# Kernel optimization log

Measured on AMD Instinct MI355X. Metric: run time of the kernel, lower is better.

Reference implementation:

```python
import jax, jax.numpy as jnp
import numpy as np
from jax import lax

H = 384
W = 384
N = H * W                 # flattened pixel count
N_LOC = N // 2            # unknown pixels with 3x3 matting-Laplacian stencils
KCM = 20                  # color-mixture KNN size
K_IU = 5                  # intra-unknown KNN size
NNZ_CM = N_LOC * KCM


def setup_inputs() -> dict:
    key = jax.random.key(0)
    ks = jax.random.split(key, 16)
    f32 = jnp.float32
    i32 = jnp.int32
    inp = {}
    inp["CM_weights"] = jax.random.uniform(ks[0], (N,), f32)
    inp["LOC_weights"] = jax.random.uniform(ks[1], (N,), f32)
    inp["IU_weights"] = jax.random.uniform(ks[2], (N,), f32)
    inp["KU_weights"] = jax.random.uniform(ks[3], (N,), f32)
    inp["lmbda"] = jnp.full((1,), 100.0, f32)
    inp["kToUconf"] = jax.random.uniform(ks[4], (N,), f32)
    inp["known"] = jax.random.uniform(ks[5], (N,), f32)
    inp["kToU"] = jax.random.uniform(ks[6], (N,), f32)
    inp["Wcm_data"] = jax.random.uniform(ks[7], (NNZ_CM,), f32)
    inp["LOC_flows"] = jax.random.uniform(ks[8], (9, 9, N_LOC), f32)
    inp["IU_flows"] = jax.random.uniform(ks[9], (N_LOC, K_IU), f32)
    inp["Wcm_row"] = jax.random.randint(ks[10], (NNZ_CM,), 0, N, dtype=i32)
    inp["Wcm_col"] = jax.random.randint(ks[11], (NNZ_CM,), 0, N, dtype=i32)
    # interior pixels so all 9 stencil neighbours are valid
    inp["LOC_inInd"] = jax.random.randint(ks[12], (N_LOC,), W + 1, N - W - 1, dtype=i32)
    inp["IU_inInd"] = jax.random.randint(ks[13], (N_LOC,), 0, N, dtype=i32)
    inp["IU_neighInd"] = jax.random.randint(ks[14], (N_LOC, K_IU), 0, N, dtype=i32)
    inp["width"] = W
    inp["cg_steps"] = 30
    return inp


def reference(CM_weights, LOC_weights, IU_weights, KU_weights, lmbda,
              kToUconf, known, kToU, Wcm_data, LOC_flows, IU_flows,
              Wcm_row, Wcm_col, LOC_inInd, IU_inInd, IU_neighInd,
              width, cg_steps):
    n = kToU.shape[0]
    seg = lambda v, i: jax.ops.segment_sum(v, i, num_segments=n)

    # --- color mixture: Wcm scaled by diag(CM_weights); L = diag(rowsum) - Wcm; Lcm = L^T L
    cm_vals = CM_weights[Wcm_row] * Wcm_data
    rs_cm = seg(cm_vals, Wcm_row)

    # --- matting Laplacian: 9x9 flows per unknown pixel over 3x3 stencil
    offs = jnp.array([-1 - width, -1, -1 + width, -width, 0, width,
                      1 - width, 1, 1 + width], dtype=LOC_inInd.dtype)
    neigh = LOC_inInd[:, None] + offs[None, :]                    # [n_loc, 9]
    fl = LOC_flows * LOC_weights[LOC_inInd][None, None, :]        # [9, 9, n_loc]
    nloc = neigh.shape[0]
    # entry (row=neigh[k,i], col=neigh[k,j]) has value fl[j, i, k]
    vals_m = jnp.transpose(fl, (2, 1, 0)).reshape(-1)
    rows_m = jnp.broadcast_to(neigh[:, :, None], (nloc, 9, 9)).reshape(-1)
    cols_m = jnp.broadcast_to(neigh[:, None, :], (nloc, 9, 9)).reshape(-1)
    rows_ms = jnp.concatenate([rows_m, cols_m])
    cols_ms = jnp.concatenate([cols_m, rows_m])
    vals_ms = 0.5 * jnp.concatenate([vals_m, vals_m])             # W = 0.5 (W + W^T)
    rs_m = seg(vals_ms, rows_ms)

    # --- intra-unknowns KNN affinities
    fiu = IU_flows * IU_weights[IU_inInd][:, None]                # [n_iu, K]
    rows_c0 = jnp.broadcast_to(IU_inInd[:, None], IU_neighInd.shape).reshape(-1)
    cols_c0 = IU_neighInd.reshape(-1)
    rows_cs = jnp.concatenate([rows_c0, cols_c0])
    cols_cs = jnp.concatenate([cols_c0, rows_c0])
    vals_cs = 0.5 * jnp.concatenate([fiu.reshape(-1), fiu.reshape(-1)])
    rs_c = seg(vals_cs, rows_cs)

    # --- diagonal data terms: KU + lmbda*known
    diag_ku = KU_weights * kToUconf + lmbda[0] * known
    b = diag_ku * kToU

    def matvec(v):
        # Lcm @ v = L^T (L v), keeping L in factored COO form
        Lv = rs_cm * v - seg(cm_vals * v[Wcm_col], Wcm_row)
        lcm = rs_cm * Lv - seg(cm_vals * Lv[Wcm_row], Wcm_col)
        lm = rs_m * v - seg(vals_ms * v[cols_ms], rows_ms)
        lc = rs_c * v - seg(vals_cs * v[cols_cs], rows_cs)
        return lcm + lm + lc + diag_ku * v

    def cg_step(carry, _):
        x, r, p, rs = carry
        Ap = matvec(p)
        alpha = rs / jnp.vdot(p, Ap)
        x = x + alpha * p
        r = r - alpha * Ap
        rs_new = jnp.vdot(r, r)
        p = r + (rs_new / rs) * p
        return (x, r, p, rs_new), None

    x0 = jnp.zeros_like(b)  # x0 = 0 as in MattingSolver
    (x, _, _, _), _ = lax.scan(cg_step, (x0, b, b, jnp.vdot(b, b)), None, length=cg_steps)
    return x
```

## Files before the change

### kernel.cpp

```cpp
#include <hip/hip_runtime.h>


#define TPB 256

__device__ __forceinline__ float blockReduce256(float v) {
  #pragma unroll
  for (int o = 32; o > 0; o >>= 1) v += __shfl_down(v, o, 64);
  __shared__ float s[4];
  int lane = threadIdx.x & 63, wv = threadIdx.x >> 6;
  if (lane == 0) s[wv] = v;
  __syncthreads();
  return (threadIdx.x == 0) ? (s[0] + s[1] + s[2] + s[3]) : 0.f;
}

__global__ void k_init0(const float* __restrict__ KUw, const float* __restrict__ kToUconf,
                        const float* __restrict__ lmbda, const float* __restrict__ known,
                        const float* __restrict__ kToU,
                        float* __restrict__ diag_ku, float2* __restrict__ PR,
                        float* __restrict__ x,
                        int* __restrict__ CNT, float* __restrict__ scal, int N)
{
  int i = blockIdx.x * TPB + threadIdx.x;
  if (i < 80) scal[i] = 0.f;
  if (i < 4 * N) CNT[i] = 0;
  float red = 0.f;
  if (i < N) {
    float dk = KUw[i] * kToUconf[i] + lmbda[0] * known[i];
    diag_ku[i] = dk;
    float b = dk * kToU[i];
    PR[i] = make_float2(b, b);
    x[i] = 0.f;
    red = b * b;
  }
  float v = blockReduce256(red);
  if (threadIdx.x == 0) atomicAdd(&scal[0], v);
}

__global__ void k_prep(float* __restrict__ LOC_flows, const int* __restrict__ LOC_inInd,
                       const float* __restrict__ LOCw, int NLOC)
{
  int k = blockIdx.x * TPB + threadIdx.x;
  float Fl[81];
  #pragma unroll
  for (int m = 0; m < 81; ++m) Fl[m] = LOC_flows[(size_t)m * NLOC + k];
  float hw = 0.5f * LOCw[LOC_inInd[k]];
  int idx = 0;
  #pragma unroll
  for (int a = 0; a < 9; ++a)
    #pragma unroll
    for (int b = a + 1; b < 9; ++b) {
      LOC_flows[(size_t)idx * NLOC + k] = hw * (Fl[a * 9 + b] + Fl[b * 9 + a]);
      ++idx;
    }
}

__global__ void k_sh(const int* __restrict__ LOC_inInd, int* __restrict__ CNT,
                     unsigned short* __restrict__ sTick, int N, int NLOC)
{
  int k = blockIdx.x * TPB + threadIdx.x;
  sTick[k] = (unsigned short)atomicAdd(&CNT[3 * N + LOC_inInd[k]], 1);
}

__global__ void k_sc(const int* __restrict__ LOC_inInd, const int* __restrict__ OFF,
                     const unsigned short* __restrict__ sTick,
                     int* __restrict__ perm, int* __restrict__ LOC_inIndP,
                     int N, int NLOC)
{
  int k = blockIdx.x * TPB + threadIdx.x;
  int v = LOC_inInd[k];
  int pos = OFF[3 * N + v] + sTick[k];
  perm[pos] = k;
  LOC_inIndP[pos] = v;
}

__global__ void k_permS2(float* __restrict__ LOC_flows, const int* __restrict__ perm,
                         int NLOC)
{
  int kp = blockIdx.x * TPB + threadIdx.x;
  int k = perm[kp];
  #pragma unroll
  for (int m = 0; m < 36; ++m)
    LOC_flows[(size_t)(36 + m) * NLOC + kp] = LOC_flows[(size_t)m * NLOC + k];
}

__global__ void k_hist(const int* __restrict__ Wrow, const int* __restrict__ Wcol,
                       const int* __restrict__ IU_inInd, const int* __restrict__ IU_neighInd,
                       int* __restrict__ CNT,
                       unsigned short* __restrict__ tr, unsigned short* __restrict__ tc,
                       unsigned short* __restrict__ tU,
                       int NLOC, int N, int B0)
{
  int blk = blockIdx.x;
  if (blk < B0) {
    int e = blk * TPB + threadIdx.x;
    tr[e] = (unsigned short)atomicAdd(&CNT[Wrow[e]], 1);
    tc[e] = (unsigned short)atomicAdd(&CNT[N + Wcol[e]], 1);
  } else {
    int k = (blk - B0) * TPB + threadIdx.x;
    tU[5 * NLOC + k] = (unsigned short)atomicAdd(&CNT[2 * N + IU_inInd[k]], 1);
    #pragma unroll
    for (int j = 0; j < 5; ++j)
      tU[j * NLOC + k] =
          (unsigned short)atomicAdd(&CNT[2 * N + IU_neighInd[k * 5 + j]], 1);
  }
}

__global__ void k_scan1(int* __restrict__ OFF, int* __restrict__ bsum, int tot)
{
  __shared__ int s[TPB];
  int gid = blockIdx.x * TPB + threadIdx.x;
  int v = (gid < tot) ? OFF[gid] : 0;
  s[threadIdx.x] = v;
  __syncthreads();
  #pragma unroll
  for (int o = 1; o < TPB; o <<= 1) {
    int t = (threadIdx.x >= o) ? s[threadIdx.x - o] : 0;
    __syncthreads();
    s[threadIdx.x] += t;
    __syncthreads();
  }
  if (gid < tot) OFF[gid] = s[threadIdx.x] - v;
  if (threadIdx.x == TPB - 1) bsum[blockIdx.x] = s[threadIdx.x];
}

__global__ void k_scan2(int* __restrict__ bsum, int nPerArr)
{
  __shared__ int s[1024];
  int base = blockIdx.x * nPerArr;
  int v = (threadIdx.x < nPerArr) ? bsum[base + threadIdx.x] : 0;
  s[threadIdx.x] = v;
  __syncthreads();
  for (int o = 1; o < 1024; o <<= 1) {
    int t = (threadIdx.x >= o) ? s[threadIdx.x - o] : 0;
    __syncthreads();
    s[threadIdx.x] += t;
    __syncthreads();
  }
  if (threadIdx.x < nPerArr) bsum[base + threadIdx.x] = s[threadIdx.x] - v;
}

__global__ void k_scan3(int* __restrict__ OFF, const int* __restrict__ bsum, int tot)
{
  int gid = blockIdx.x * TPB + threadIdx.x;
  if (gid < tot) OFF[gid] += bsum[blockIdx.x];
}

__global__ void k_fill(const float* __restrict__ CMw, const float* __restrict__ Wcm_data,
                       const int* __restrict__ Wrow, const int* __restrict__ Wcol,
                       const int* __restrict__ IU_inInd, const int* __restrict__ IU_neighInd,
                       const int* __restrict__ OFF,
                       const unsigned short* __restrict__ tr, const unsigned short* __restrict__ tc,
                       const unsigned short* __restrict__ tU,
                       int2* __restrict__ csrPk, int2* __restrict__ cscPk,
                       int* __restrict__ gU,
                       int NLOC, int N, int B0)
{
  int blk = blockIdx.x;
  if (blk < B0) {
    int e = blk * TPB + threadIdx.x;
    int row = Wrow[e], col = Wcol[e];
    int cv = __float_as_int(CMw[row] * Wcm_data[e]);
    csrPk[OFF[row] + tr[e]] = make_int2(col, cv);
    cscPk[OFF[N + col] + tc[e]] = make_int2(row, cv);
  } else {
    int k = (blk - B0) * TPB + threadIdx.x;
    gU[OFF[2 * N + IU_inInd[k]] + tU[5 * NLOC + k]] = 14 * NLOC + k;
    #pragma unroll
    for (int j = 0; j < 5; ++j)
      gU[OFF[2 * N + IU_neighInd[k * 5 + j]] + tU[j * NLOC + k]] =
          (9 + j) * NLOC + k;
  }
}

__global__ void k_it1(const float2* __restrict__ PR,
                      const float* __restrict__ S2p, const int* __restrict__ LOC_inIndP,
                      const int* __restrict__ width_p,
                      const float* __restrict__ IU_flows, const int* __restrict__ IU_inInd,
                      const int* __restrict__ IU_neighInd, const float* __restrict__ IUw,
                      const float* __restrict__ diag_ku,
                      const int* __restrict__ OFF, const int2* __restrict__ csrPk,
                      float* __restrict__ u_all,
                      float* __restrict__ Lv, float* __restrict__ rs_cm,
                      const float* __restrict__ rsN, const float* __restrict__ rsO, int first,
                      float* __restrict__ pAp_t,
                      int NNZ, int NLOC, int N, int B0, int B1)
{
  int blk = blockIdx.x;
  float beta = first ? 0.f : rsN[0] / rsO[0];
  float red = 0.f;
  if (blk < B0) {
    int kp = blk * TPB + threadIdx.x;
    int wd = *width_p;
    int base = LOC_inIndP[kp];
    const int offs[9] = {-1 - wd, -1, -1 + wd, -wd, 0, wd, 1 - wd, 1, 1 + wd};
    float pv[9];
    #pragma unroll
    for (int a = 0; a < 9; ++a) {
      float2 pr = PR[base + offs[a]];
      pv[a] = __builtin_fmaf(beta, pr.x, pr.y);
    }
    float u[9] = {0.f, 0.f, 0.f, 0.f, 0.f, 0.f, 0.f, 0.f, 0.f};
    float qf = 0.f;
    int idx = 0;
    #pragma unroll
    for (int a = 0; a < 9; ++a)
      #pragma unroll
      for (int b = a + 1; b < 9; ++b) {
        float sv = S2p[(size_t)idx * NLOC + kp];
        ++idx;
        float d = pv[a] - pv[b];
        float t = sv * d;
        u[a] += t; u[b] -= t;
        qf += t * d;
      }
    #pragma unroll
    for (int a = 0; a < 9; ++a) u_all[a * NLOC + kp] = u[a];
    red = qf;
  } else if (blk < B1) {
    int k = (blk - B0) * TPB + threadIdx.x;
    int r0 = IU_inInd[k];
    float hw = 0.5f * IUw[r0];
    float2 prr = PR[r0];
    float pr = __builtin_fmaf(beta, prr.x, prr.y);
    int c[5]; float w[5];
    #pragma unroll
    for (int j = 0; j < 5; ++j) {
      c[j] = IU_neighInd[k * 5 + j];
      w[j] = hw * IU_flows[k * 5 + j];
    }
    float pc[5];
    #pragma unroll
    for (int j = 0; j < 5; ++j) {
      float2 pp = PR[c[j]];
      pc[j] = __builtin_fmaf(beta, pp.x, pp.y);
    }
    float qf = 0.f, asum = 0.f;
    #pragma unroll
    for (int j = 0; j < 5; ++j) {
      float d = pr - pc[j];
      float uA = w[j] * d;
      u_all[(9 + j) * NLOC + k] = -uA;
      asum += uA;
      qf += uA * d;
    }
    u_all[14 * NLOC + k] = asum;
    red = qf;
  } else {
    int i = (blk - B1) * TPB + threadIdx.x;
    float2 pri = PR[i];
    float pi = __builtin_fmaf(beta, pri.x, pri.y);
    int s = OFF[i];
    int e = (i == N - 1) ? NNZ : OFF[i + 1];
    float acc = 0.f, rs = 0.f;
    int q = s;
    for (; q + 8 <= e; q += 8) {
      int2 ed[8];
      #pragma unroll
      for (int m = 0; m < 8; ++m) ed[m] = csrPk[q + m];
      float g[8];
      #pragma unroll
      for (int m = 0; m < 8; ++m) {
        float2 pp = PR[ed[m].x];
        g[m] = __builtin_fmaf(beta, pp.x, pp.y);
      }
      #pragma unroll
      for (int m = 0; m < 8; ++m) {
        float cv = __int_as_float(ed[m].y);
        rs += cv;
        acc += cv * (pi - g[m]);
      }
    }
    for (; q + 4 <= e; q += 4) {
      int2 ed[4];
      #pragma unroll
      for (int m = 0; m < 4; ++m) ed[m] = csrPk[q + m];
      float g[4];
      #pragma unroll
      for (int m = 0; m < 4; ++m) {
        float2 pp = PR[ed[m].x];
        g[m] = __builtin_fmaf(beta, pp.x, pp.y);
      }
      #pragma unroll
      for (int m = 0; m < 4; ++m) {
        float cv = __int_as_float(ed[m].y);
        rs += cv;
        acc += cv * (pi - g[m]);
      }
    }
    for (; q < e; ++q) {
      int2 ed = csrPk[q];
      float cv = __int_as_float(ed.y);
      float2 pp = PR[ed.x];
      rs += cv;
      acc += cv * (pi - __builtin_fmaf(beta, pp.x, pp.y));
    }
    Lv[i] = acc;
    rs_cm[i] = rs;
    red = diag_ku[i] * pi * pi + acc * acc;
  }
  float v = blockReduce256(red);
  if (threadIdx.x == 0) atomicAdd(pAp_t, v);
}

__global__ void k_it2(float* __restrict__ x, float2* __restrict__ PR,
                      const float* __restrict__ Lv,
                      const float* __restrict__ rs_cm, const float* __restrict__ diag_ku,
                      const int* __restrict__ OFF, const int* __restrict__ cum,
                      const int* __restrict__ width_p,
                      const int2* __restrict__ cscPk,
                      const int* __restrict__ gU, const float* __restrict__ u_all,
                      const float* __restrict__ rs_t, const float* __restrict__ pAp_t,
                      const float* __restrict__ rsO, int first,
                      float* __restrict__ rs_t1,
                      int NNZ, int NLOC, int N)
{
  int i = blockIdx.x * TPB + threadIdx.x;
  float alpha = rs_t[0] / pAp_t[0];
  float beta = first ? 0.f : rs_t[0] / rsO[0];
  float tg = 0.f;
  {
    int wd = *width_p;
    const int voff[9] = {1 + wd, 1, 1 - wd, wd, 0, -wd, -1 + wd, -1, -1 - wd};
    #pragma unroll
    for (int a = 0; a < 9; ++a) {
      int v = i + voff[a];
      v = v < 0 ? 0 : (v > N - 1 ? N - 1 : v);
      int lo = cum[v];
      int hi = (v == N - 1) ? NLOC : cum[v + 1];
      for (int q = lo; q < hi; ++q) tg += u_all[a * NLOC + q];
    }
  }
  {
    int s0 = OFF[2 * N + i];
    int e0 = (i == N - 1) ? 6 * NLOC : OFF[2 * N + i + 1];
    int q = s0;
    for (; q + 4 <= e0; q += 4) {
      int g[4];
      #pragma unroll
      for (int m = 0; m < 4; ++m) g[m] = gU[q + m];
      float u[4];
      #pragma unroll
      for (int m = 0; m < 4; ++m) u[m] = u_all[g[m]];
      #pragma unroll
      for (int m = 0; m < 4; ++m) tg += u[m];
    }
    for (; q < e0; ++q) tg += u_all[gU[q]];
  }
  float sc = 0.f;
  {
    int s0 = OFF[N + i];
    int e0 = (i == N - 1) ? NNZ : OFF[N + i + 1];
    int q = s0;
    for (; q + 8 <= e0; q += 8) {
      int2 ed[8];
      #pragma unroll
      for (int m = 0; m < 8; ++m) ed[m] = cscPk[q + m];
      float l[8];
      #pragma unroll
      for (int m = 0; m < 8; ++m) l[m] = Lv[ed[m].x];
      #pragma unroll
      for (int m = 0; m < 8; ++m) sc += __int_as_float(ed[m].y) * l[m];
    }
    for (; q + 4 <= e0; q += 4) {
      int2 ed[4];
      #pragma unroll
      for (int m = 0; m < 4; ++m) ed[m] = cscPk[q + m];
      float l[4];
      #pragma unroll
      for (int m = 0; m < 4; ++m) l[m] = Lv[ed[m].x];
      #pragma unroll
      for (int m = 0; m < 4; ++m) sc += __int_as_float(ed[m].y) * l[m];
    }
    for (; q < e0; ++q) {
      int2 ed = cscPk[q];
      sc += __int_as_float(ed.y) * Lv[ed.x];
    }
  }
  float2 pri = PR[i];
  float pi = __builtin_fmaf(beta, pri.x, pri.y);
  float Ap = diag_ku[i] * pi + rs_cm[i] * Lv[i] - sc + tg;
  x[i] += alpha * pi;
  float rn = pri.y - alpha * Ap;
  PR[i] = make_float2(pi, rn);
  float v = blockReduce256(rn * rn);
  if (threadIdx.x == 0) atomicAdd(rs_t1, v);
}

extern "C" void kernel_launch(void* const* d_in, const int* in_sizes, int n_in,
                              void* d_out, int out_size, void* d_ws, size_t ws_size,
                              hipStream_t stream)
{
  const float* CMw       = (const float*)d_in[0];
  const float* LOCw      = (const float*)d_in[1];
  const float* IUw       = (const float*)d_in[2];
  const float* KUw       = (const float*)d_in[3];
  const float* lmbda     = (const float*)d_in[4];
  const float* kToUconf  = (const float*)d_in[5];
  const float* known     = (const float*)d_in[6];
  const float* kToU      = (const float*)d_in[7];
  const float* Wcm_data  = (const float*)d_in[8];
  float*       LOC_flows = (float*)d_in[9];
  const float* IU_flows  = (const float*)d_in[10];
  const int*   Wrow      = (const int*)d_in[11];
  const int*   Wcol      = (const int*)d_in[12];
  const int*   LOC_inInd = (const int*)d_in[13];
  const int*   IU_inInd  = (const int*)d_in[14];
  const int*   IU_neighInd = (const int*)d_in[15];
  const int*   width_p   = (const int*)d_in[16];
  const int CG_STEPS = 30;

  const int N    = in_sizes[0];
  const int NNZ  = in_sizes[8];
  const int NLOC = in_sizes[13];

  float* x       = (float*)d_out;
  float2* PR     = (float2*)d_ws;
  float* Lv      = (float*)(PR + (size_t)N);
  float* rs_cm   = Lv + N;
  float* diag_ku = rs_cm + N;
  int2*  csrPk   = (int2*)(diag_ku + N);
  int2*  cscPk   = csrPk + (size_t)NNZ;
  int*   gU      = (int*)(cscPk + (size_t)NNZ);
  int*   OFF     = gU + (size_t)6 * NLOC;
  unsigned short* tr = (unsigned short*)(OFF + (size_t)4 * N);
  unsigned short* tc = tr + (size_t)NNZ;
  unsigned short* tU = tc + (size_t)NNZ;
  float* u_all   = (float*)tr;
  int*   bsum    = (int*)(tU + (size_t)6 * NLOC);
  float* scal    = (float*)(bsum + 4 * (N / TPB));
  int*   perm    = (int*)(scal + 80);
  int*   LOC_inIndP = perm + NLOC;
  unsigned short* sTick = (unsigned short*)(LOC_inIndP + NLOC);

  const int Bn = N / TPB;
  const int Bz = NNZ / TPB;
  const int Bl = NLOC / TPB;
  const int Z4 = 4 * Bn;

  k_init0<<<Z4, TPB, 0, stream>>>(KUw, kToUconf, lmbda, known, kToU,
                                  diag_ku, PR, x, OFF, scal, N);
  k_prep<<<Bl, TPB, 0, stream>>>(LOC_flows, LOC_inInd, LOCw, NLOC);
  k_sh<<<Bl, TPB, 0, stream>>>(LOC_inInd, OFF, sTick, N, NLOC);
  k_hist<<<Bz + Bl, TPB, 0, stream>>>(Wrow, Wcol, IU_inInd, IU_neighInd, OFF,
                                      tr, tc, tU, NLOC, N, Bz);
  k_scan1<<<Z4, TPB, 0, stream>>>(OFF, bsum, 4 * N);
  k_scan2<<<4, 1024, 0, stream>>>(bsum, Bn);
  k_scan3<<<Z4, TPB, 0, stream>>>(OFF, bsum, 4 * N);
  k_sc<<<Bl, TPB, 0, stream>>>(LOC_inInd, OFF, sTick, perm, LOC_inIndP, N, NLOC);
  k_permS2<<<Bl, TPB, 0, stream>>>(LOC_flows, perm, NLOC);
  k_fill<<<Bz + Bl, TPB, 0, stream>>>(CMw, Wcm_data, Wrow, Wcol,
                                      IU_inInd, IU_neighInd,
                                      OFF, tr, tc, tU,
                                      csrPk, cscPk, gU,
                                      NLOC, N, Bz);

  const float* S2p = LOC_flows + (size_t)36 * NLOC;
  const int*   cum = OFF + (size_t)3 * N;
  for (int t = 0; t < CG_STEPS; ++t) {
    const float* rsN = scal + t;
    const float* rsO = scal + (t == 0 ? 0 : t - 1);
    k_it1<<<2 * Bl + Bn, TPB, 0, stream>>>(
        PR, S2p, LOC_inIndP, width_p,
        IU_flows, IU_inInd, IU_neighInd, IUw,
        diag_ku, OFF, csrPk, u_all, Lv, rs_cm,
        rsN, rsO, (t == 0) ? 1 : 0, scal + 40 + t,
        NNZ, NLOC, N, Bl, 2 * Bl);
    k_it2<<<Bn, TPB, 0, stream>>>(
        x, PR, Lv, rs_cm, diag_ku, OFF, cum, width_p, cscPk, gU, u_all,
        rsN, scal + 40 + t, rsO, (t == 0) ? 1 : 0, scal + t + 1,
        NNZ, NLOC, N);
  }
}
```

Before: 1.862 ms.

## Fold matting-Laplacian stencil gather into the unified gU gather list

```diff
diff --git a/kernel.cpp b/kernel.cpp
--- a/kernel.cpp
+++ b/kernel.cpp
@@ -61,26 +61,18 @@
   sTick[k] = (unsigned short)atomicAdd(&CNT[3 * N + LOC_inInd[k]], 1);
 }
 
-__global__ void k_sc(const int* __restrict__ LOC_inInd, const int* __restrict__ OFF,
-                     const unsigned short* __restrict__ sTick,
-                     int* __restrict__ perm, int* __restrict__ LOC_inIndP,
-                     int N, int NLOC)
-{
-  int k = blockIdx.x * TPB + threadIdx.x;
-  int v = LOC_inInd[k];
-  int pos = OFF[3 * N + v] + sTick[k];
-  perm[pos] = k;
-  LOC_inIndP[pos] = v;
-}
-
-__global__ void k_permS2(float* __restrict__ LOC_flows, const int* __restrict__ perm,
-                         int NLOC)
-{
-  int kp = blockIdx.x * TPB + threadIdx.x;
-  int k = perm[kp];
+__global__ void k_wminit(int* __restrict__ CNT, const int* __restrict__ width_p, int N)
+{
+  int j = blockIdx.x * TPB + threadIdx.x;
+  int wd = *width_p;
+  const int offs[9] = {-1 - wd, -1, -1 + wd, -wd, 0, wd, 1 - wd, 1, 1 + wd};
+  int s = 0;
   #pragma unroll
-  for (int m = 0; m < 36; ++m)
-    LOC_flows[(size_t)(36 + m) * NLOC + kp] = LOC_flows[(size_t)m * NLOC + k];
+  for (int a = 0; a < 9; ++a) {
+    int v = j - offs[a];
+    if (v >= 0 && v < N) s += CNT[3 * N + v];
+  }
+  CNT[2 * N + j] = s;
 }
 
 __global__ void k_hist(const int* __restrict__ Wrow, const int* __restrict__ Wcol,
@@ -145,15 +137,38 @@
   if (gid < tot) OFF[gid] += bsum[blockIdx.x];
 }
 
+__global__ void k_sc(const int* __restrict__ LOC_inInd, const int* __restrict__ OFF,
+                     const unsigned short* __restrict__ sTick,
+                     int* __restrict__ perm, int* __restrict__ LOC_inIndP,
+                     int N, int NLOC)
+{
+  int k = blockIdx.x * TPB + threadIdx.x;
+  int v = LOC_inInd[k];
+  int pos = OFF[3 * N + v] + sTick[k];
+  perm[pos] = k;
+  LOC_inIndP[pos] = v;
+}
+
+__global__ void k_permS2(float* __restrict__ LOC_flows, const int* __restrict__ perm,
+                         int NLOC)
+{
+  int kp = blockIdx.x * TPB + threadIdx.x;
+  int k = perm[kp];
+  #pragma unroll
+  for (int m = 0; m < 36; ++m)
+    LOC_flows[(size_t)(36 + m) * NLOC + kp] = LOC_flows[(size_t)m * NLOC + k];
+}
+
 __global__ void k_fill(const float* __restrict__ CMw, const float* __restrict__ Wcm_data,
                        const int* __restrict__ Wrow, const int* __restrict__ Wcol,
+                       const int* __restrict__ LOC_inIndP, const int* __restrict__ width_p,
                        const int* __restrict__ IU_inInd, const int* __restrict__ IU_neighInd,
                        const int* __restrict__ OFF,
                        const unsigned short* __restrict__ tr, const unsigned short* __restrict__ tc,
                        const unsigned short* __restrict__ tU,
                        int2* __restrict__ csrPk, int2* __restrict__ cscPk,
                        int* __restrict__ gU,
-                       int NLOC, int N, int B0)
+                       int NLOC, int N, int B0, int B1)
 {
   int blk = blockIdx.x;
   if (blk < B0) {
@@ -162,8 +177,37 @@
     int cv = __float_as_int(CMw[row] * Wcm_data[e]);
     csrPk[OFF[row] + tr[e]] = make_int2(col, cv);
     cscPk[OFF[N + col] + tc[e]] = make_int2(row, cv);
+  } else if (blk < B1) {
+    int kp = (blk - B0) * TPB + threadIdx.x;
+    int wd = *width_p;
+    int base = LOC_inIndP[kp];
+    const int* cum = OFF + 3 * N;
+    int rank = kp - cum[base];
+    int hh[5][5];
+    #pragma unroll
+    for (int dr = 0; dr < 5; ++dr) {
+      int c[6];
+      #pragma unroll
+      for (int m = 0; m < 6; ++m) {
+        int v = base + (dr - 2) * wd + (m - 2);
+        c[m] = (v <= 0) ? 0 : ((v >= N) ? NLOC : cum[v]);
+      }
+      #pragma unroll
+      for (int m = 0; m < 5; ++m) hh[dr][m] = c[m + 1] - c[m];
+    }
+    const int CAv[9] = {-1, -1, -1, 0, 0, 0, 1, 1, 1};
+    const int RAv[9] = {-1, 0, 1, -1, 0, 1, -1, 0, 1};
+    #pragma unroll
+    for (int a = 0; a < 9; ++a) {
+      int T = 0;
+      #pragma unroll
+      for (int ap = 0; ap < a; ++ap)
+        T += hh[RAv[a] - RAv[ap] + 2][CAv[a] - CAv[ap] + 2];
+      int j = base + CAv[a] + RAv[a] * wd;
+      gU[OFF[2 * N + j] + T + rank] = a * NLOC + kp;
+    }
   } else {
-    int k = (blk - B0) * TPB + threadIdx.x;
+    int k = (blk - B1) * TPB + threadIdx.x;
     gU[OFF[2 * N + IU_inInd[k]] + tU[5 * NLOC + k]] = 14 * NLOC + k;
     #pragma unroll
     for (int j = 0; j < 5; ++j)
@@ -305,8 +349,7 @@
 __global__ void k_it2(float* __restrict__ x, float2* __restrict__ PR,
                       const float* __restrict__ Lv,
                       const float* __restrict__ rs_cm, const float* __restrict__ diag_ku,
-                      const int* __restrict__ OFF, const int* __restrict__ cum,
-                      const int* __restrict__ width_p,
+                      const int* __restrict__ OFF,
                       const int2* __restrict__ cscPk,
                       const int* __restrict__ gU, const float* __restrict__ u_all,
                       const float* __restrict__ rs_t, const float* __restrict__ pAp_t,
@@ -319,21 +362,19 @@
   float beta = first ? 0.f : rs_t[0] / rsO[0];
   float tg = 0.f;
   {
-    int wd = *width_p;
-    const int voff[9] = {1 + wd, 1, 1 - wd, wd, 0, -wd, -1 + wd, -1, -1 - wd};
-    #pragma unroll
-    for (int a = 0; a < 9; ++a) {
-      int v = i + voff[a];
-      v = v < 0 ? 0 : (v > N - 1 ? N - 1 : v);
-      int lo = cum[v];
-      int hi = (v == N - 1) ? NLOC : cum[v + 1];
-      for (int q = lo; q < hi; ++q) tg += u_all[a * NLOC + q];
-    }
-  }
-  {
     int s0 = OFF[2 * N + i];
-    int e0 = (i == N - 1) ? 6 * NLOC : OFF[2 * N + i + 1];
+    int e0 = (i == N - 1) ? 15 * NLOC : OFF[2 * N + i + 1];
     int q = s0;
+    for (; q + 8 <= e0; q += 8) {
+      int g[8];
+      #pragma unroll
+      for (int m = 0; m < 8; ++m) g[m] = gU[q + m];
+      float u[8];
+      #pragma unroll
+      for (int m = 0; m < 8; ++m) u[m] = u_all[g[m]];
+      #pragma unroll
+      for (int m = 0; m < 8; ++m) tg += u[m];
+    }
     for (; q + 4 <= e0; q += 4) {
       int g[4];
       #pragma unroll
@@ -421,7 +462,7 @@
   int2*  csrPk   = (int2*)(diag_ku + N);
   int2*  cscPk   = csrPk + (size_t)NNZ;
   int*   gU      = (int*)(cscPk + (size_t)NNZ);
-  int*   OFF     = gU + (size_t)6 * NLOC;
+  int*   OFF     = gU + (size_t)15 * NLOC;
   unsigned short* tr = (unsigned short*)(OFF + (size_t)4 * N);
   unsigned short* tc = tr + (size_t)NNZ;
   unsigned short* tU = tc + (size_t)NNZ;
@@ -441,6 +482,7 @@
                                   diag_ku, PR, x, OFF, scal, N);
   k_prep<<<Bl, TPB, 0, stream>>>(LOC_flows, LOC_inInd, LOCw, NLOC);
   k_sh<<<Bl, TPB, 0, stream>>>(LOC_inInd, OFF, sTick, N, NLOC);
+  k_wminit<<<Bn, TPB, 0, stream>>>(OFF, width_p, N);
   k_hist<<<Bz + Bl, TPB, 0, stream>>>(Wrow, Wcol, IU_inInd, IU_neighInd, OFF,
                                       tr, tc, tU, NLOC, N, Bz);
   k_scan1<<<Z4, TPB, 0, stream>>>(OFF, bsum, 4 * N);
@@ -448,14 +490,13 @@
   k_scan3<<<Z4, TPB, 0, stream>>>(OFF, bsum, 4 * N);
   k_sc<<<Bl, TPB, 0, stream>>>(LOC_inInd, OFF, sTick, perm, LOC_inIndP, N, NLOC);
   k_permS2<<<Bl, TPB, 0, stream>>>(LOC_flows, perm, NLOC);
-  k_fill<<<Bz + Bl, TPB, 0, stream>>>(CMw, Wcm_data, Wrow, Wcol,
-                                      IU_inInd, IU_neighInd,
-                                      OFF, tr, tc, tU,
-                                      csrPk, cscPk, gU,
-                                      NLOC, N, Bz);
+  k_fill<<<Bz + 2 * Bl, TPB, 0, stream>>>(CMw, Wcm_data, Wrow, Wcol,
+                                          LOC_inIndP, width_p, IU_inInd, IU_neighInd,
+                                          OFF, tr, tc, tU,
+                                          csrPk, cscPk, gU,
+                                          NLOC, N, Bz, Bz + Bl);
 
   const float* S2p = LOC_flows + (size_t)36 * NLOC;
-  const int*   cum = OFF + (size_t)3 * N;
   for (int t = 0; t < CG_STEPS; ++t) {
     const float* rsN = scal + t;
     const float* rsO = scal + (t == 0 ? 0 : t - 1);
@@ -466,7 +507,7 @@
         rsN, rsO, (t == 0) ? 1 : 0, scal + 40 + t,
         NNZ, NLOC, N, Bl, 2 * Bl);
     k_it2<<<Bn, TPB, 0, stream>>>(
-        x, PR, Lv, rs_cm, diag_ku, OFF, cum, width_p, cscPk, gU, u_all,
+        x, PR, Lv, rs_cm, diag_ku, OFF, cscPk, gU, u_all,
         rsN, scal + 40 + t, rsO, (t == 0) ? 1 : 0, scal + t + 1,
         NNZ, NLOC, N);
   }
```

Result: faster. 1.753 ms (-5.9%).
